# Kernel optimization log

Hardware: AMD Instinct MI355X
Metric: run time of the kernel (lower is better)

Reference implementation:

```python
import jax, jax.numpy as jnp
import numpy as np
from jax import lax

MASK_EPS = 1e-45  # matches torch (mask + 1e-45).log()

B, N, L, T = 32, 64, 64, 10
V, D, H = 50257, 256, 512


def setup_inputs() -> dict:
    key = jax.random.key(0)
    ks = jax.random.split(key, 10)
    s = 0.02
    return {
        "sents": jax.random.randint(ks[0], (B, N, L), 0, V),
        "titles": jax.random.randint(ks[1], (B, N, T), 0, V),
        "emb": jax.random.normal(ks[2], (V, D), jnp.float32) * s,
        "Wt": jax.random.normal(ks[3], (D, H), jnp.float32) * s,
        "bt": jnp.zeros((H,), jnp.float32),
        "W_ih": jax.random.normal(ks[4], (D, 3 * H), jnp.float32) * s,
        "W_hh": jax.random.normal(ks[5], (H, 3 * H), jnp.float32) * s,
        "b_ih": jnp.zeros((3 * H,), jnp.float32),
        "b_hh": jnp.zeros((3 * H,), jnp.float32),
        "W_att_in": jax.random.normal(ks[6], (H, H), jnp.float32) * s,
        "W_att_out": jax.random.normal(ks[7], (2 * H, H), jnp.float32) * s,
        "b_att_out": jnp.zeros((H,), jnp.float32),
    }


def reference(sents, titles, emb, Wt, bt, W_ih, W_hh, b_ih, b_hh,
              W_att_in, W_att_out, b_att_out):
    # embedding gather + per-sentence bag-of-words sum  [B,N,D]
    x = emb[sents].sum(axis=2)
    # title -> initial sentence-level hidden (t2h), titles[:,0,:-2] summed
    h0 = emb[titles[:, 0]].sum(axis=1) @ Wt + bt            # [B,H]

    def gru_step(h, xi):
        gi = xi @ W_ih + b_ih                               # [B,3H]
        gh = h @ W_hh + b_hh
        ir, iz, inn = jnp.split(gi, 3, axis=-1)
        hr, hz, hn = jnp.split(gh, 3, axis=-1)
        r = jax.nn.sigmoid(ir + hr)
        z = jax.nn.sigmoid(iz + hz)
        n = jnp.tanh(inn + r * hn)
        h_new = (1.0 - z) * n + z * h
        return h_new, h_new

    _, hs = lax.scan(gru_step, h0, jnp.swapaxes(x, 0, 1))   # [N,B,H]
    hs = jnp.swapaxes(hs, 0, 1)                             # [B,N,H]

    # GlobalAttention over the growing stack of hs with incremental mask
    # == causal attention over sentence hidden states
    q = hs @ W_att_in                                       # [B,N,H]
    align = jnp.einsum('bqh,bkh->bqk', q, hs)               # [B,N,N]
    causal = jnp.tril(jnp.ones((N, N), jnp.float32))
    align = align + jnp.log(causal + MASK_EPS)
    a = jax.nn.softmax(align, axis=-1)
    c = jnp.einsum('bqk,bkh->bqh', a, hs)                   # [B,N,H]
    attn_h = jnp.tanh(jnp.concatenate([c, hs], axis=-1) @ W_att_out + b_att_out)
    return attn_h
```

## Files before the change

kernel.cpp:

```cpp
#include <hip/hip_runtime.h>
#include <hip/hip_bf16.h>

constexpr int cB = 32, cN = 64, cL = 64, cT = 10, cD = 256, cH = 512, cH3 = 1536;
constexpr int cBN = cB * cN;
constexpr int cNP1 = cN + 1;

typedef __bf16 bf16x8 __attribute__((ext_vector_type(8)));
typedef float f32x4 __attribute__((ext_vector_type(4)));

__device__ __forceinline__ ushort f2bf(float f) {
  __hip_bfloat16 h = __float2bfloat16(f);
  return *reinterpret_cast<ushort*>(&h);
}

__global__ void k_embed_x(const int* __restrict__ sents, const float* __restrict__ emb,
                          float* __restrict__ x) {
  __shared__ int idx[cL];
  int bn = blockIdx.x, t = threadIdx.x;
  if (t < cL) idx[t] = sents[bn * cL + t];
  __syncthreads();
  float acc = 0.f;
#pragma unroll 8
  for (int l = 0; l < cL; ++l) acc += emb[(long)idx[l] * cD + t];
  x[bn * cD + t] = acc;
}

__global__ void k_title(const int* __restrict__ titles, const float* __restrict__ emb,
                        float* __restrict__ tsum) {
  __shared__ int idx[cT];
  int b = blockIdx.x, t = threadIdx.x;
  if (t < cT) idx[t] = titles[b * cN * cT + t];
  __syncthreads();
  float acc = 0.f;
#pragma unroll
  for (int i = 0; i < cT; ++i) acc += emb[(long)idx[i] * cD + t];
  tsum[b * cD + t] = acc;
}

__global__ void k_h0(const float* __restrict__ tsum, const float* __restrict__ Wt,
                     const float* __restrict__ bt, float* __restrict__ hse) {
  int i = blockIdx.x * blockDim.x + threadIdx.x;
  int b = i >> 9, hh = i & (cH - 1);
  const float* ts = tsum + b * cD;
  float acc = bt[hh];
  for (int k = 0; k < cD; ++k) acc += ts[k] * Wt[(long)k * cH + hh];
  hse[(long)b * cNP1 * cH + hh] = acc;
}

__global__ void k_xcast(const float* __restrict__ x, ushort* __restrict__ xb) {
  int bn = blockIdx.x, t = threadIdx.x;
  float4 v = ((const float4*)(x + (long)bn * cD))[t];
  ushort4 o;
  o.x = f2bf(v.x); o.y = f2bf(v.y); o.z = f2bf(v.z); o.w = f2bf(v.w);
  *(ushort4*)(xb + (long)bn * cD + t * 4) = o;
}

__global__ void k_bti(const float* __restrict__ W, ushort* __restrict__ Bt) {
  __shared__ float tile[64][65];
  int col0 = blockIdx.x * 64, k0 = blockIdx.y * 64;
  int t = threadIdx.x;
  for (int i = t; i < 4096; i += 256) {
    int kr = i >> 6, cc = i & 63;
    tile[kr][cc] = W[(long)(k0 + kr) * cH3 + col0 + cc];
  }
  __syncthreads();
  for (int i = t; i < 4096; i += 256) {
    int cc = i >> 6, kr = i & 63;
    Bt[(long)(col0 + cc) * cD + k0 + kr] = f2bf(tile[kr][cc]);
  }
}

__global__ void k_bq(const float* __restrict__ W, ushort* __restrict__ Bt) {
  __shared__ float tile[64][65];
  int col0 = blockIdx.x * 64, k0 = blockIdx.y * 64;
  int t = threadIdx.x;
  for (int i = t; i < 4096; i += 256) {
    int kr = i >> 6, cc = i & 63;
    tile[kr][cc] = W[(long)(k0 + kr) * cH + col0 + cc];
  }
  __syncthreads();
  for (int i = t; i < 4096; i += 256) {
    int cc = i >> 6, kr = i & 63;
    Bt[(long)(col0 + cc) * cH + k0 + kr] = f2bf(tile[kr][cc]);
  }
}

__global__ void __launch_bounds__(256) k_gi_mfma(
    const ushort* __restrict__ xb, const ushort* __restrict__ Bt,
    const float* __restrict__ b_ih, float* __restrict__ gi) {
  __shared__ char lds[16384];
  int bn0 = blockIdx.x * 64, col0 = blockIdx.y * 64;
  int t = threadIdx.x;
  int w = t >> 6, lane = t & 63;
  f32x4 acc[4];
#pragma unroll
  for (int i = 0; i < 4; ++i) acc[i] = (f32x4){0.f, 0.f, 0.f, 0.f};
  int r = lane & 15, kg = lane >> 4;
  for (int kc = 0; kc < 4; ++kc) {
    int k0 = kc * 64;
#pragma unroll
    for (int p = 0; p < 2; ++p) {
      int i = t + p * 256;
      int row = i >> 3, ks = i & 7;
      float4 va = *(const float4*)(xb + (long)(bn0 + row) * cD + k0 + ks * 8);
      *(float4*)(lds + ((row * 128 + ks * 16) ^ ((row & 7) << 4))) = va;
      float4 vb = *(const float4*)(Bt + (long)(col0 + row) * cD + k0 + ks * 8);
      *(float4*)(lds + 8192 + ((row * 128 + ks * 16) ^ ((row & 7) << 4))) = vb;
    }
    __syncthreads();
#pragma unroll
    for (int s = 0; s < 2; ++s) {
      int arow = w * 16 + r;
      bf16x8 a = *(const bf16x8*)(lds + ((arow * 128 + s * 64 + kg * 16) ^ ((arow & 7) << 4)));
#pragma unroll
      for (int cf = 0; cf < 4; ++cf) {
        int bcol = cf * 16 + r;
        bf16x8 bb = *(const bf16x8*)(lds + 8192 +
                                     ((bcol * 128 + s * 64 + kg * 16) ^ ((bcol & 7) << 4)));
        acc[cf] = __builtin_amdgcn_mfma_f32_16x16x32_bf16(a, bb, acc[cf], 0, 0, 0);
      }
    }
    __syncthreads();
  }
  int rq = lane >> 4;
#pragma unroll
  for (int cf = 0; cf < 4; ++cf) {
    int col = col0 + cf * 16 + r;
    float bv = b_ih[col];
#pragma unroll
    for (int reg = 0; reg < 4; ++reg) {
      int row = bn0 + w * 16 + rq * 4 + reg;
      gi[(long)row * cH3 + col] = acc[cf][reg] + bv;
    }
  }
}

__global__ void __launch_bounds__(512, 1) k_gru_step(
    const float* __restrict__ gi, const float* __restrict__ W_hh,
    const float* __restrict__ b_hh, float* __restrict__ hse, int step) {
  __shared__ float part[512][13];
  int cg = blockIdx.x & 31;
  int bg = blockIdx.x >> 5;
  int t = threadIdx.x;

  float ir = 0.f, iz = 0.f, in_ = 0.f, bhr = 0.f, bhz = 0.f, bhn = 0.f, hold = 0.f;
  int e_bl = (t >> 4) & 3, e_cl = t & 15;
  if (t < 64) {
    int bb = bg * 4 + e_bl;
    int hh = cg * 16 + e_cl;
    long girow = ((long)bb * cN + step) * cH3;
    ir = gi[girow + hh];
    iz = gi[girow + hh + cH];
    in_ = gi[girow + hh + 2 * cH];
    bhr = b_hh[hh];
    bhz = b_hh[hh + cH];
    bhn = b_hh[hh + 2 * cH];
    hold = hse[((long)bb * cNP1 + step) * cH + hh];
  }

  int c4 = t & 3, b = (t >> 2) & 3, kp = t >> 4;
  int col0 = cg * 16 + c4 * 4;
  const float* hrow = hse + ((long)(bg * 4 + b) * cNP1 + step) * cH;
  int k0 = kp * 16;
  float4 h0 = *(const float4*)(hrow + k0);
  float4 h1 = *(const float4*)(hrow + k0 + 4);
  float4 h2 = *(const float4*)(hrow + k0 + 8);
  float4 h3 = *(const float4*)(hrow + k0 + 12);
  float ar[4] = {0, 0, 0, 0}, az[4] = {0, 0, 0, 0}, an[4] = {0, 0, 0, 0};
#define GRU_K(HV, KOFF)                                                         \
  {                                                                             \
    const float* wp = W_hh + (long)(k0 + (KOFF)) * cH3 + col0;                  \
    float4 wr = *(const float4*)(wp);                                           \
    float4 wz = *(const float4*)(wp + cH);                                      \
    float4 wn = *(const float4*)(wp + 2 * cH);                                  \
    ar[0] += (HV)*wr.x; ar[1] += (HV)*wr.y; ar[2] += (HV)*wr.z; ar[3] += (HV)*wr.w; \
    az[0] += (HV)*wz.x; az[1] += (HV)*wz.y; az[2] += (HV)*wz.z; az[3] += (HV)*wz.w; \
    an[0] += (HV)*wn.x; an[1] += (HV)*wn.y; an[2] += (HV)*wn.z; an[3] += (HV)*wn.w; \
  }
  GRU_K(h0.x, 0) GRU_K(h0.y, 1) GRU_K(h0.z, 2) GRU_K(h0.w, 3)
  GRU_K(h1.x, 4) GRU_K(h1.y, 5) GRU_K(h1.z, 6) GRU_K(h1.w, 7)
  GRU_K(h2.x, 8) GRU_K(h2.y, 9) GRU_K(h2.z, 10) GRU_K(h2.w, 11)
  GRU_K(h3.x, 12) GRU_K(h3.y, 13) GRU_K(h3.z, 14) GRU_K(h3.w, 15)
#undef GRU_K
#pragma unroll
  for (int j = 0; j < 4; ++j) {
    part[t][j] = ar[j];
    part[t][4 + j] = az[j];
    part[t][8 + j] = an[j];
  }
  __syncthreads();
  if (t < 64) {
    int c4f = e_cl >> 2, jf = e_cl & 3;
    float sr = 0.f, sz = 0.f, sn = 0.f;
#pragma unroll
    for (int p = 0; p < 32; ++p) {
      const float* pp = part[p * 16 + e_bl * 4 + c4f];
      sr += pp[jf];
      sz += pp[4 + jf];
      sn += pp[8 + jf];
    }
    int bb = bg * 4 + e_bl;
    int hh = cg * 16 + e_cl;
    float rr = 1.f / (1.f + __expf(-(ir + sr + bhr)));
    float zz = 1.f / (1.f + __expf(-(iz + sz + bhz)));
    float nn = tanhf(in_ + rr * (sn + bhn));
    hse[((long)bb * cNP1 + step + 1) * cH + hh] = (1.f - zz) * nn + zz * hold;
  }
}

__global__ void k_hscast(const float* __restrict__ hse, ushort* __restrict__ hsb) {
  int bn = blockIdx.x, t = threadIdx.x;
  int b = bn >> 6, n = bn & 63;
  float4 v = ((const float4*)(hse + ((long)b * cNP1 + 1 + n) * cH))[t];
  ushort4 o;
  o.x = f2bf(v.x); o.y = f2bf(v.y); o.z = f2bf(v.z); o.w = f2bf(v.w);
  *(ushort4*)(hsb + (long)bn * cH + t * 4) = o;
}

__global__ void __launch_bounds__(256) k_q_mfma(
    const ushort* __restrict__ hsb, const ushort* __restrict__ Bt,
    float* __restrict__ q) {
  __shared__ char lds[16384];
  int bn0 = blockIdx.x * 64, col0 = blockIdx.y * 64;
  int t = threadIdx.x;
  int w = t >> 6, lane = t & 63;
  f32x4 acc[4];
#pragma unroll
  for (int i = 0; i < 4; ++i) acc[i] = (f32x4){0.f, 0.f, 0.f, 0.f};
  int r = lane & 15, kg = lane >> 4;
  for (int kc = 0; kc < 8; ++kc) {
    int k0 = kc * 64;
#pragma unroll
    for (int p = 0; p < 2; ++p) {
      int i = t + p * 256;
      int row = i >> 3, ks = i & 7;
      float4 va = *(const float4*)(hsb + (long)(bn0 + row) * cH + k0 + ks * 8);
      *(float4*)(lds + ((row * 128 + ks * 16) ^ ((row & 7) << 4))) = va;
      float4 vb = *(const float4*)(Bt + (long)(col0 + row) * cH + k0 + ks * 8);
      *(float4*)(lds + 8192 + ((row * 128 + ks * 16) ^ ((row & 7) << 4))) = vb;
    }
    __syncthreads();
#pragma unroll
    for (int s = 0; s < 2; ++s) {
      int arow = w * 16 + r;
      bf16x8 a = *(const bf16x8*)(lds + ((arow * 128 + s * 64 + kg * 16) ^ ((arow & 7) << 4)));
#pragma unroll
      for (int cf = 0; cf < 4; ++cf) {
        int bcol = cf * 16 + r;
        bf16x8 bb = *(const bf16x8*)(lds + 8192 +
                                     ((bcol * 128 + s * 64 + kg * 16) ^ ((bcol & 7) << 4)));
        acc[cf] = __builtin_amdgcn_mfma_f32_16x16x32_bf16(a, bb, acc[cf], 0, 0, 0);
      }
    }
    __syncthreads();
  }
  int rq = lane >> 4;
#pragma unroll
  for (int cf = 0; cf < 4; ++cf) {
    int col = col0 + cf * 16 + r;
#pragma unroll
    for (int reg = 0; reg < 4; ++reg) {
      int row = bn0 + w * 16 + rq * 4 + reg;
      q[(long)row * cH + col] = acc[cf][reg];
    }
  }
}

__global__ void k_attn(const float* __restrict__ q, const float* __restrict__ hse,
                       float* __restrict__ c) {
  __shared__ float qs[cH];
  __shared__ float part[256];
  __shared__ float aw[cN];
  int bn = blockIdx.x;
  int b = bn >> 6, n = bn & 63;
  int t = threadIdx.x;
  qs[t] = q[(long)bn * cH + t];
  qs[t + 256] = q[(long)bn * cH + t + 256];
  __syncthreads();
  int k = t & 63;
  int p = t >> 6;
  const float* hrow = hse + ((long)b * cNP1 + 1 + k) * cH + p * 128;
  float s = 0.f;
#pragma unroll 8
  for (int j = 0; j < 128; ++j) s += qs[p * 128 + j] * hrow[j];
  part[t] = s;
  __syncthreads();
  if (t < 64) {
    float sc = part[t] + part[t + 64] + part[t + 128] + part[t + 192];
    if (t > n) sc = -1e30f;
    float m = sc;
#pragma unroll
    for (int off = 32; off; off >>= 1) m = fmaxf(m, __shfl_xor(m, off));
    float e = __expf(sc - m);
    float sum = e;
#pragma unroll
    for (int off = 32; off; off >>= 1) sum += __shfl_xor(sum, off);
    aw[t] = e / sum;
  }
  __syncthreads();
  float c0 = 0.f, c1 = 0.f;
  for (int kk = 0; kk < cN; ++kk) {
    float a = aw[kk];
    const float* hr = hse + ((long)b * cNP1 + 1 + kk) * cH;
    c0 += a * hr[t];
    c1 += a * hr[t + 256];
  }
  c[(long)bn * cH + t] = c0;
  c[(long)bn * cH + t + 256] = c1;
}

__global__ void k_cat(const float* __restrict__ c, const float* __restrict__ hse,
                      ushort* __restrict__ cat) {
  int bn = blockIdx.x, t = threadIdx.x;
  int b = bn >> 6, n = bn & 63;
  float4 v = (t < 128) ? ((const float4*)(c + (long)bn * cH))[t]
                       : ((const float4*)(hse + ((long)b * cNP1 + 1 + n) * cH))[t - 128];
  ushort4 o;
  o.x = f2bf(v.x); o.y = f2bf(v.y); o.z = f2bf(v.z); o.w = f2bf(v.w);
  *(ushort4*)(cat + (long)bn * 1024 + t * 4) = o;
}

__global__ void k_bt(const float* __restrict__ W, ushort* __restrict__ Bt) {
  int t = threadIdx.x;
  int col = blockIdx.x * 2 + (t >> 7);
  int kg = t & 127;
  ushort u[8];
#pragma unroll
  for (int j = 0; j < 8; ++j) u[j] = f2bf(W[(long)(kg * 8 + j) * cH + col]);
  int4 o;
  o.x = (int)u[0] | ((int)u[1] << 16);
  o.y = (int)u[2] | ((int)u[3] << 16);
  o.z = (int)u[4] | ((int)u[5] << 16);
  o.w = (int)u[6] | ((int)u[7] << 16);
  *(int4*)(Bt + (long)col * 1024 + kg * 8) = o;
}

__global__ void __launch_bounds__(256) k_out_mfma(
    const ushort* __restrict__ cat, const ushort* __restrict__ Bt,
    const float* __restrict__ bias, float* __restrict__ out) {
  __shared__ char lds[16384];
  int bn0 = blockIdx.x * 64, col0 = blockIdx.y * 64;
  int t = threadIdx.x;
  int w = t >> 6, lane = t & 63;
  f32x4 acc[4];
#pragma unroll
  for (int i = 0; i < 4; ++i) acc[i] = (f32x4){0.f, 0.f, 0.f, 0.f};
  int r = lane & 15, kg = lane >> 4;
  for (int kc = 0; kc < 16; ++kc) {
    int k0 = kc * 64;
#pragma unroll
    for (int p = 0; p < 2; ++p) {
      int i = t + p * 256;
      int row = i >> 3, ks = i & 7;
      float4 va = *(const float4*)(cat + (long)(bn0 + row) * 1024 + k0 + ks * 8);
      *(float4*)(lds + ((row * 128 + ks * 16) ^ ((row & 7) << 4))) = va;
      float4 vb = *(const float4*)(Bt + (long)(col0 + row) * 1024 + k0 + ks * 8);
      *(float4*)(lds + 8192 + ((row * 128 + ks * 16) ^ ((row & 7) << 4))) = vb;
    }
    __syncthreads();
#pragma unroll
    for (int s = 0; s < 2; ++s) {
      int arow = w * 16 + r;
      bf16x8 a = *(const bf16x8*)(lds + ((arow * 128 + s * 64 + kg * 16) ^ ((arow & 7) << 4)));
#pragma unroll
      for (int cf = 0; cf < 4; ++cf) {
        int bcol = cf * 16 + r;
        bf16x8 bb = *(const bf16x8*)(lds + 8192 +
                                     ((bcol * 128 + s * 64 + kg * 16) ^ ((bcol & 7) << 4)));
        acc[cf] = __builtin_amdgcn_mfma_f32_16x16x32_bf16(a, bb, acc[cf], 0, 0, 0);
      }
    }
    __syncthreads();
  }
  int rq = lane >> 4;
#pragma unroll
  for (int cf = 0; cf < 4; ++cf) {
    int col = col0 + cf * 16 + r;
    float bv = bias[col];
#pragma unroll
    for (int reg = 0; reg < 4; ++reg) {
      int row = bn0 + w * 16 + rq * 4 + reg;
      out[(long)row * cH + col] = tanhf(acc[cf][reg] + bv);
    }
  }
}

extern "C" void kernel_launch(void* const* d_in, const int* in_sizes, int n_in,
                              void* d_out, int out_size, void* d_ws, size_t ws_size,
                              hipStream_t stream) {
  const int* sents = (const int*)d_in[0];
  const int* titles = (const int*)d_in[1];
  const float* emb = (const float*)d_in[2];
  const float* Wt = (const float*)d_in[3];
  const float* bt = (const float*)d_in[4];
  const float* W_ih = (const float*)d_in[5];
  const float* W_hh = (const float*)d_in[6];
  const float* b_ih = (const float*)d_in[7];
  const float* b_hh = (const float*)d_in[8];
  const float* W_att_in = (const float*)d_in[9];
  const float* W_att_out = (const float*)d_in[10];
  const float* b_att_out = (const float*)d_in[11];
  float* out = (float*)d_out;

  float* ws = (float*)d_ws;
  float* x = ws;
  float* tsum = x + (long)cBN * cD;
  float* gi = tsum + (long)cB * cD;
  float* hse = gi + (long)cBN * cH3;
  float* c = hse + (long)cB * cNP1 * cH;
  ushort* xb = (ushort*)(c + (long)cBN * cH);
  ushort* bti = xb + (long)cBN * cD;
  ushort* bq = bti + (long)cH3 * cD;
  float* q = gi;
  ushort* catb = (ushort*)(gi + (long)cBN * cH);
  ushort* Btb = catb + (long)cBN * 1024;
  ushort* hsb = Btb + (long)cH * 1024;

  k_embed_x<<<cBN, 256, 0, stream>>>(sents, emb, x);
  k_title<<<cB, 256, 0, stream>>>(titles, emb, tsum);
  k_h0<<<(cB * cH) / 256, 256, 0, stream>>>(tsum, Wt, bt, hse);
  k_xcast<<<cBN, 64, 0, stream>>>(x, xb);
  k_bti<<<dim3(24, 4), 256, 0, stream>>>(W_ih, bti);
  k_bq<<<dim3(8, 8), 256, 0, stream>>>(W_att_in, bq);
  k_gi_mfma<<<dim3(32, 24), 256, 0, stream>>>(xb, bti, b_ih, gi);
  for (int step = 0; step < cN; ++step)
    k_gru_step<<<256, 512, 0, stream>>>(gi, W_hh, b_hh, hse, step);
  k_hscast<<<cBN, 128, 0, stream>>>(hse, hsb);
  k_q_mfma<<<dim3(32, 8), 256, 0, stream>>>(hsb, bq, q);
  k_attn<<<cBN, 256, 0, stream>>>(q, hse, c);
  k_bt<<<256, 256, 0, stream>>>(W_att_out, Btb);
  k_cat<<<cBN, 256, 0, stream>>>(c, hse, catb);
  k_out_mfma<<<dim3(32, 8), 256, 0, stream>>>(catb, Btb, b_att_out, out);
}
```

Measured before the change: 498.9 us.

## Fuse casts into producers and batch causal attention over four queries per block

The embedding kernel now writes bf16 directly, so the separate cast kernel is gone. The hidden-state cast also writes the second half of the concat buffer. Attention is rewritten to process four queries per block, skip keys beyond the causal limit, and emit bf16 context straight into the concat buffer, which removes the concat kernel. This cuts launches, intermediate fp32 buffers and redundant hidden-state reads, at the cost of fewer attention blocks and higher per-block register and LDS use.

```diff
diff --git a/kernel.cpp b/kernel.cpp
--- a/kernel.cpp
+++ b/kernel.cpp
@@ -14,7 +14,7 @@
 }
 
 __global__ void k_embed_x(const int* __restrict__ sents, const float* __restrict__ emb,
-                          float* __restrict__ x) {
+                          ushort* __restrict__ xb) {
   __shared__ int idx[cL];
   int bn = blockIdx.x, t = threadIdx.x;
   if (t < cL) idx[t] = sents[bn * cL + t];
@@ -22,7 +22,7 @@
   float acc = 0.f;
 #pragma unroll 8
   for (int l = 0; l < cL; ++l) acc += emb[(long)idx[l] * cD + t];
-  x[bn * cD + t] = acc;
+  xb[bn * cD + t] = f2bf(acc);
 }
 
 __global__ void k_title(const int* __restrict__ titles, const float* __restrict__ emb,
@@ -45,14 +45,6 @@
   float acc = bt[hh];
   for (int k = 0; k < cD; ++k) acc += ts[k] * Wt[(long)k * cH + hh];
   hse[(long)b * cNP1 * cH + hh] = acc;
-}
-
-__global__ void k_xcast(const float* __restrict__ x, ushort* __restrict__ xb) {
-  int bn = blockIdx.x, t = threadIdx.x;
-  float4 v = ((const float4*)(x + (long)bn * cD))[t];
-  ushort4 o;
-  o.x = f2bf(v.x); o.y = f2bf(v.y); o.z = f2bf(v.z); o.w = f2bf(v.w);
-  *(ushort4*)(xb + (long)bn * cD + t * 4) = o;
 }
 
 __global__ void k_bti(const float* __restrict__ W, ushort* __restrict__ Bt) {
@@ -208,13 +200,15 @@
   }
 }
 
-__global__ void k_hscast(const float* __restrict__ hse, ushort* __restrict__ hsb) {
+__global__ void k_hscast(const float* __restrict__ hse, ushort* __restrict__ hsb,
+                         ushort* __restrict__ catb) {
   int bn = blockIdx.x, t = threadIdx.x;
   int b = bn >> 6, n = bn & 63;
   float4 v = ((const float4*)(hse + ((long)b * cNP1 + 1 + n) * cH))[t];
   ushort4 o;
   o.x = f2bf(v.x); o.y = f2bf(v.y); o.z = f2bf(v.z); o.w = f2bf(v.w);
   *(ushort4*)(hsb + (long)bn * cH + t * 4) = o;
+  *(ushort4*)(catb + (long)bn * 1024 + 512 + t * 4) = o;
 }
 
 __global__ void __launch_bounds__(256) k_q_mfma(
@@ -266,58 +260,72 @@
   }
 }
 
-__global__ void k_attn(const float* __restrict__ q, const float* __restrict__ hse,
-                       float* __restrict__ c) {
-  __shared__ float qs[cH];
-  __shared__ float part[256];
-  __shared__ float aw[cN];
-  int bn = blockIdx.x;
-  int b = bn >> 6, n = bn & 63;
-  int t = threadIdx.x;
-  qs[t] = q[(long)bn * cH + t];
-  qs[t + 256] = q[(long)bn * cH + t + 256];
-  __syncthreads();
-  int k = t & 63;
-  int p = t >> 6;
-  const float* hrow = hse + ((long)b * cNP1 + 1 + k) * cH + p * 128;
-  float s = 0.f;
-#pragma unroll 8
-  for (int j = 0; j < 128; ++j) s += qs[p * 128 + j] * hrow[j];
-  part[t] = s;
+__global__ void k_attn2(const float* __restrict__ q, const float* __restrict__ hse,
+                        ushort* __restrict__ catb) {
+  __shared__ float qs[4][cH];
+  __shared__ float part[256][5];
+  __shared__ float aw[4][cN];
+  int b = blockIdx.x, qg = blockIdx.y;
+  int n0 = qg * 4;
+  int kmax = n0 + 3;
+  int t = threadIdx.x;
+  for (int i = t; i < 4 * 128; i += 256) {
+    int g = i >> 7, j = i & 127;
+    ((float4*)qs[g])[j] = ((const float4*)(q + (long)(b * 64 + n0 + g) * cH))[j];
+  }
+  __syncthreads();
+  int k = t & 63, p = t >> 6;
+  float s0 = 0.f, s1 = 0.f, s2 = 0.f, s3 = 0.f;
+  if (k <= kmax) {
+    const float* hrow = hse + ((long)b * cNP1 + 1 + k) * cH + p * 128;
+    const float* q0 = &qs[0][p * 128];
+    const float* q1 = &qs[1][p * 128];
+    const float* q2 = &qs[2][p * 128];
+    const float* q3 = &qs[3][p * 128];
+#pragma unroll 4
+    for (int j = 0; j < 128; ++j) {
+      float hv = hrow[j];
+      s0 += q0[j] * hv;
+      s1 += q1[j] * hv;
+      s2 += q2[j] * hv;
+      s3 += q3[j] * hv;
+    }
+  }
+  part[t][0] = s0; part[t][1] = s1; part[t][2] = s2; part[t][3] = s3;
   __syncthreads();
   if (t < 64) {
-    float sc = part[t] + part[t + 64] + part[t + 128] + part[t + 192];
-    if (t > n) sc = -1e30f;
-    float m = sc;
-#pragma unroll
-    for (int off = 32; off; off >>= 1) m = fmaxf(m, __shfl_xor(m, off));
-    float e = __expf(sc - m);
-    float sum = e;
-#pragma unroll
-    for (int off = 32; off; off >>= 1) sum += __shfl_xor(sum, off);
-    aw[t] = e / sum;
-  }
-  __syncthreads();
-  float c0 = 0.f, c1 = 0.f;
-  for (int kk = 0; kk < cN; ++kk) {
-    float a = aw[kk];
+#pragma unroll
+    for (int g = 0; g < 4; ++g) {
+      float sc = part[t][g] + part[t + 64][g] + part[t + 128][g] + part[t + 192][g];
+      if (t > n0 + g) sc = -1e30f;
+      float m = sc;
+#pragma unroll
+      for (int off = 32; off; off >>= 1) m = fmaxf(m, __shfl_xor(m, off));
+      float e = __expf(sc - m);
+      float sum = e;
+#pragma unroll
+      for (int off = 32; off; off >>= 1) sum += __shfl_xor(sum, off);
+      aw[g][t] = e / sum;
+    }
+  }
+  __syncthreads();
+  float c0[4] = {0, 0, 0, 0}, c1[4] = {0, 0, 0, 0};
+  for (int kk = 0; kk <= kmax; ++kk) {
     const float* hr = hse + ((long)b * cNP1 + 1 + kk) * cH;
-    c0 += a * hr[t];
-    c1 += a * hr[t + 256];
-  }
-  c[(long)bn * cH + t] = c0;
-  c[(long)bn * cH + t + 256] = c1;
-}
-
-__global__ void k_cat(const float* __restrict__ c, const float* __restrict__ hse,
-                      ushort* __restrict__ cat) {
-  int bn = blockIdx.x, t = threadIdx.x;
-  int b = bn >> 6, n = bn & 63;
-  float4 v = (t < 128) ? ((const float4*)(c + (long)bn * cH))[t]
-                       : ((const float4*)(hse + ((long)b * cNP1 + 1 + n) * cH))[t - 128];
-  ushort4 o;
-  o.x = f2bf(v.x); o.y = f2bf(v.y); o.z = f2bf(v.z); o.w = f2bf(v.w);
-  *(ushort4*)(cat + (long)bn * 1024 + t * 4) = o;
+    float h0 = hr[t], h1 = hr[t + 256];
+#pragma unroll
+    for (int g = 0; g < 4; ++g) {
+      float a = aw[g][kk];
+      c0[g] += a * h0;
+      c1[g] += a * h1;
+    }
+  }
+#pragma unroll
+  for (int g = 0; g < 4; ++g) {
+    long row = (long)(b * 64 + n0 + g) * 1024;
+    catb[row + t] = f2bf(c0[g]);
+    catb[row + t + 256] = f2bf(c1[g]);
+  }
 }
 
 __global__ void k_bt(const float* __restrict__ W, ushort* __restrict__ Bt) {
@@ -416,19 +424,17 @@
   ushort* Btb = catb + (long)cBN * 1024;
   ushort* hsb = Btb + (long)cH * 1024;
 
-  k_embed_x<<<cBN, 256, 0, stream>>>(sents, emb, x);
+  k_embed_x<<<cBN, 256, 0, stream>>>(sents, emb, xb);
   k_title<<<cB, 256, 0, stream>>>(titles, emb, tsum);
   k_h0<<<(cB * cH) / 256, 256, 0, stream>>>(tsum, Wt, bt, hse);
-  k_xcast<<<cBN, 64, 0, stream>>>(x, xb);
   k_bti<<<dim3(24, 4), 256, 0, stream>>>(W_ih, bti);
   k_bq<<<dim3(8, 8), 256, 0, stream>>>(W_att_in, bq);
   k_gi_mfma<<<dim3(32, 24), 256, 0, stream>>>(xb, bti, b_ih, gi);
   for (int step = 0; step < cN; ++step)
     k_gru_step<<<256, 512, 0, stream>>>(gi, W_hh, b_hh, hse, step);
-  k_hscast<<<cBN, 128, 0, stream>>>(hse, hsb);
+  k_hscast<<<cBN, 128, 0, stream>>>(hse, hsb, catb);
   k_q_mfma<<<dim3(32, 8), 256, 0, stream>>>(hsb, bq, q);
-  k_attn<<<cBN, 256, 0, stream>>>(q, hse, c);
+  k_attn2<<<dim3(cB, 16), 256, 0, stream>>>(q, hse, catb);
   k_bt<<<256, 256, 0, stream>>>(W_att_out, Btb);
-  k_cat<<<cBN, 256, 0, stream>>>(c, hse, catb);
   k_out_mfma<<<dim3(32, 8), 256, 0, stream>>>(catb, Btb, b_att_out, out);
 }
```

Result: faster. 461.7 us (-7.4%).
